# Optimization experiments

Hardware: AMD Instinct MI355X
Metric: run time of the kernel (lower is better)

Reference implementation:

```python
import jax, jax.numpy as jnp
import numpy as np
import math

D = 128       # d_model (file-scope constant)
L_LEN = 128   # length; forced == d_model by the un-transposed attention call
NH = 4        # n_head
DK = D // NH
K = 7         # depthwise conv kernel size
LC = 4        # conv_num
EPS = 1e-5    # LayerNorm eps
NEG = -1e30


def _pos_encoding():
    i = np.arange(D).astype(np.float64)
    freqs = np.where(i % 2 == 0, 10000.0 ** (-i / D), -(10000.0 ** ((1 - i) / D)))
    phases = np.where(i % 2 == 0, 0.0, math.pi / 2)
    pos = np.arange(L_LEN).astype(np.float64)[None, :]          # (1, L)
    pe = np.sin(pos * freqs[:, None] + phases[:, None])          # (D, L)
    return jnp.asarray(pe, jnp.float32)

PE = _pos_encoding()


def layernorm2d(x, w, b):
    # LayerNorm over the trailing (D, L) dims jointly, elementwise affine (D, L)
    mu = x.mean(axis=(-2, -1), keepdims=True)
    var = x.var(axis=(-2, -1), keepdims=True)
    return (x - mu) * jax.lax.rsqrt(var + EPS) * w + b


def sep_conv(x, dw_w, dw_b, pw_w, pw_b):
    # depthwise conv1d (groups=C) then 1x1 pointwise conv. x: (B, C, L)
    h = jax.lax.conv_general_dilated(
        x, dw_w[:, None, :], window_strides=(1,), padding=[(K // 2, K // 2)],
        dimension_numbers=('NCH', 'OIH', 'NCH'), feature_group_count=D)
    h = h + dw_b[:, None]
    return jnp.einsum('bcl,oc->bol', h, pw_w) + pw_b[:, None]


def mha(x, mask_f, Wq, bq, Wk, bk, Wv, bv, Wo, bo):
    # x: (B, Lx, F) with Lx == F == D here (module feeds (B, d_model, length) untransposed)
    B, Lx, _ = x.shape
    q = (x @ Wq.T + bq).reshape(B, Lx, NH, DK)
    k = (x @ Wk.T + bk).reshape(B, Lx, NH, DK)
    v = (x @ Wv.T + bv).reshape(B, Lx, NH, DK)
    scores = jnp.einsum('bqhd,bkhd->bhqk', q, k) * (1.0 / math.sqrt(DK))
    m = mask_f[:, None, None, :]                         # (B,1,1,Lx)
    scores = scores * (1.0 - m) + m * NEG                # mask_logits
    attn = jax.nn.softmax(scores, axis=-1)
    out = jnp.einsum('bhqk,bkhd->bqhd', attn, v).reshape(B, Lx, D)
    return out @ Wo.T + bo


def setup_inputs() -> dict:
    key = jax.random.key(0)
    ks = jax.random.split(key, 16)
    B = 1024
    s = 0.02
    inp = {
        'x': jax.random.normal(ks[0], (B, D, L_LEN), jnp.float32),
        'mask': jax.random.randint(ks[1], (B, L_LEN), 0, 2, jnp.int32),
        'dw_w': jax.random.normal(ks[2], (LC, D, K), jnp.float32) * s,
        'dw_b': jnp.zeros((LC, D), jnp.float32),
        'pw_w': jax.random.normal(ks[3], (LC, D, D), jnp.float32) * s,
        'pw_b': jnp.zeros((LC, D), jnp.float32),
        'normb_w': jnp.ones((D, L_LEN), jnp.float32),
        'normb_b': jnp.zeros((D, L_LEN), jnp.float32),
        'norms_w': jnp.ones((LC, D, L_LEN), jnp.float32),
        'norms_b': jnp.zeros((LC, D, L_LEN), jnp.float32),
        'norme_w': jnp.ones((D, L_LEN), jnp.float32),
        'norme_b': jnp.zeros((D, L_LEN), jnp.float32),
        'Wq': jax.random.normal(ks[4], (D, D), jnp.float32) * s,
        'bq': jnp.zeros((D,), jnp.float32),
        'Wk': jax.random.normal(ks[5], (D, D), jnp.float32) * s,
        'bk': jnp.zeros((D,), jnp.float32),
        'Wv': jax.random.normal(ks[6], (D, D), jnp.float32) * s,
        'bv': jnp.zeros((D,), jnp.float32),
        'Wo': jax.random.normal(ks[7], (D, D), jnp.float32) * s,
        'bo': jnp.zeros((D,), jnp.float32),
        'fc_w': jax.random.normal(ks[8], (D, D), jnp.float32) * s,
        'fc_b': jnp.zeros((D,), jnp.float32),
    }
    return inp


def reference(x, mask, dw_w, dw_b, pw_w, pw_b, normb_w, normb_b, norms_w, norms_b,
              norme_w, norme_b, Wq, bq, Wk, bk, Wv, bv, Wo, bo, fc_w, fc_b):
    # Eval mode: all dropouts are identity.
    mask_f = mask.astype(x.dtype)
    out = x + PE                                  # PosEncoder
    res = out
    out = layernorm2d(out, normb_w, normb_b)      # normb
    for i in range(LC):                           # fixed small layer loop
        h = sep_conv(out, dw_w[i], dw_b[i], pw_w[i], pw_b[i])
        out = jax.nn.relu(h) + res
        res = out
        out = layernorm2d(out, norms_w[i], norms_b[i])
    att = mha(out, mask_f, Wq, bq, Wk, bk, Wv, bv, Wo, bo)
    out = att + res
    res = out
    out = layernorm2d(out, norme_w, norme_b)
    # fc applied over channel dim: (B,C,L)->(B,L,C) linear ->(B,C,L)
    h = jnp.einsum('bcl,oc->bol', out, fc_w) + fc_b[:, None]
    out = jax.nn.relu(h) + res
    return out
```

## Files before the change

### kernel.cpp

```cpp
#include <hip/hip_runtime.h>

#define NEGF -1e30f
#define EPSF 1e-5f

typedef __attribute__((ext_vector_type(8))) short bf16x8;
typedef __attribute__((ext_vector_type(4))) float f32x4;
typedef unsigned short u16;
typedef unsigned int u32;

#define WSU_PW 0
#define WSU_FC 65536
#define WSU_WO 81920
#define WSU_WQ 98304
#define WSU_WK 114688
#define WSU_WV 131072
#define WSU_END 147456

__device__ __forceinline__ u16 f2bf(float x) {
  u32 u = __float_as_uint(x);
  u += 0x7fffu + ((u >> 16) & 1u);
  return (u16)(u >> 16);
}
__device__ __forceinline__ float bf2f(u16 u) {
  return __uint_as_float(((u32)u) << 16);
}
__device__ __forceinline__ f32x4 mfma16(bf16x8 a, bf16x8 b, f32x4 c) {
  return __builtin_amdgcn_mfma_f32_16x16x32_bf16(a, b, c, 0, 0, 0);
}
__device__ __forceinline__ void mm_frags(const u16* base, bf16x8* f) {
  f[0] = *(const bf16x8*)(base);
  f[1] = *(const bf16x8*)(base + 32);
  f[2] = *(const bf16x8*)(base + 64);
  f[3] = *(const bf16x8*)(base + 96);
}

__global__ __launch_bounds__(128) void prep_kernel(
    const float* __restrict__ pw_w, const float* __restrict__ fc_w,
    const float* __restrict__ Wo, const float* __restrict__ Wq,
    const float* __restrict__ Wk, const float* __restrict__ Wv,
    u16* __restrict__ wsu) {
  int job = blockIdx.x, r = blockIdx.y, c = threadIdx.x;
  int idx = r * 128 + c;
  if (job < 4)       wsu[WSU_PW + job * 16384 + idx] = f2bf(pw_w[job * 16384 + idx]);
  else if (job == 4) wsu[WSU_FC + idx] = f2bf(fc_w[idx]);
  else if (job == 5) wsu[WSU_WO + idx] = f2bf(Wo[idx]);
  else if (job == 6) wsu[WSU_WQ + idx] = f2bf(Wq[idx]);
  else if (job == 7) wsu[WSU_WK + idx] = f2bf(Wk[idx]);
  else if (job == 8) wsu[WSU_WV + idx] = f2bf(Wv[idx]);
  else {
    float* pe = (float*)(wsu + WSU_END);
    int d = r, pos = c;
    double freq, phase;
    if ((d & 1) == 0) { freq = pow(10000.0, -(double)d / 128.0); phase = 0.0; }
    else { freq = -pow(10000.0, (1.0 - (double)d) / 128.0); phase = 1.5707963267948966; }
    pe[d * 128 + pos] = (float)sin((double)pos * freq + phase);
  }
}

__device__ __forceinline__ void ln_stats(const float* resv, float* red, int t,
                                         float& mu, float& inv) {
  float s = 0.f, s2 = 0.f;
#pragma unroll
  for (int i = 0; i < 16; i++) { float v = resv[i]; s += v; s2 += v * v; }
#pragma unroll
  for (int off = 32; off > 0; off >>= 1) {
    s += __shfl_down(s, off, 64);
    s2 += __shfl_down(s2, off, 64);
  }
  if ((t & 63) == 0) { red[(t >> 6) * 2] = s; red[(t >> 6) * 2 + 1] = s2; }
  __syncthreads();
  float S = 0.f, S2 = 0.f;
#pragma unroll
  for (int i = 0; i < 16; i++) { S += red[2 * i]; S2 += red[2 * i + 1]; }
  mu = S * (1.0f / 16384.0f);
  float var = S2 * (1.0f / 16384.0f) - mu * mu;
  inv = rsqrtf(var + EPSF);
}

__global__ __launch_bounds__(1024) void enc_kernel(
    const float* __restrict__ x, const int* __restrict__ mask,
    const float* __restrict__ dw_w, const float* __restrict__ dw_b,
    const float* __restrict__ pw_b,
    const float* __restrict__ normb_w, const float* __restrict__ normb_b,
    const float* __restrict__ norms_w, const float* __restrict__ norms_b,
    const float* __restrict__ norme_w, const float* __restrict__ norme_b,
    const float* __restrict__ bq, const float* __restrict__ bk,
    const float* __restrict__ bv, const float* __restrict__ bo,
    const float* __restrict__ fc_b, const u16* __restrict__ wsu,
    const float* __restrict__ pe, float* __restrict__ out) {
  __shared__ __align__(16) u16 A_raw[128 * 136 + 16];
  __shared__ __align__(16) u16 B_[21760];
  __shared__ float mask_s[128];
  __shared__ float red[32];
  u16* A = A_raw + 8;
  u16* QH = B_;
  u16* KH = B_ + 5120;
  u16* VT = B_ + 17408;
  u16* PN = B_;

  const int t = threadIdx.x;
  const int b = blockIdx.x;
  const int lane = t & 63;
  const int r16 = lane & 15;
  const int quad = lane >> 4;
  const int wv = t >> 6;
  const int m0 = __builtin_amdgcn_readfirstlane((wv >> 1) << 4);
  const int nh = __builtin_amdgcn_readfirstlane(wv & 1);
  const int l = t & 127;
  const int og = __builtin_amdgcn_readfirstlane(t >> 7);
  const int obase = og << 4;
  const int dup = __builtin_amdgcn_readfirstlane(wv >> 3);
  const int mq0 = __builtin_amdgcn_readfirstlane((wv & 7) << 4);

  if (t < 128) mask_s[t] = (float)mask[b * 128 + t];

  float res[16];
  {
    const float* xb = x + (size_t)b * 16384;
#pragma unroll
    for (int i = 0; i < 16; i++) {
      int o = obase + i;
      res[i] = xb[o * 128 + l] + pe[o * 128 + l];
    }
  }
  {
    float mu, inv;
    ln_stats(res, red, t, mu, inv);
#pragma unroll
    for (int i = 0; i < 16; i++) {
      int o = obase + i;
      A[o * 136 + l] = f2bf((res[i] - mu) * inv * normb_w[o * 128 + l] + normb_b[o * 128 + l]);
    }
    __syncthreads();
  }

#pragma unroll 1
  for (int layer = 0; layer < 4; layer++) {
    {
      const float* dwp = dw_w + layer * 896 + l * 7;
      float wreg[7];
#pragma unroll
      for (int j = 0; j < 7; j++) wreg[j] = dwp[j];
      float bias = dw_b[layer * 128 + l];
      const u16* xrow = A + l * 136;
#pragma unroll
      for (int k = 0; k < 2; k++) {
        const int lb = (og << 4) + 8 * k;
        bf16x8 vz = {0, 0, 0, 0, 0, 0, 0, 0};
        bf16x8 vc = *(const bf16x8*)(xrow + lb);
        bf16x8 vp = (lb == 0) ? vz : *(const bf16x8*)(xrow + lb - 8);
        bf16x8 vn = (lb == 120) ? vz : *(const bf16x8*)(xrow + lb + 8);
        float w14[14];
        w14[0] = bf2f((u16)vp[5]); w14[1] = bf2f((u16)vp[6]); w14[2] = bf2f((u16)vp[7]);
#pragma unroll
        for (int j = 0; j < 8; j++) w14[3 + j] = bf2f((u16)vc[j]);
        w14[11] = bf2f((u16)vn[0]); w14[12] = bf2f((u16)vn[1]); w14[13] = bf2f((u16)vn[2]);
#pragma unroll
        for (int j = 0; j < 8; j++) {
          float a = bias;
#pragma unroll
          for (int tt = 0; tt < 7; tt++) a += w14[j + tt] * wreg[tt];
          B_[(lb + j) * 136 + l] = f2bf(a);
        }
      }
    }
    __syncthreads();
    {
      const u16* pwp = wsu + WSU_PW + (layer << 14) + (m0 + r16) * 128 + quad * 8;
      bf16x8 a[4];
      mm_frags(pwp, a);
#pragma unroll
      for (int ni = 0; ni < 4; ni++) {
        int n = nh * 4 + ni;
        const u16* hb = B_ + (16 * n + r16) * 136 + quad * 8;
        f32x4 c = {0.f, 0.f, 0.f, 0.f};
        c = mfma16(a[0], *(const bf16x8*)(hb), c);
        c = mfma16(a[1], *(const bf16x8*)(hb + 32), c);
        c = mfma16(a[2], *(const bf16x8*)(hb + 64), c);
        c = mfma16(a[3], *(const bf16x8*)(hb + 96), c);
        u16* sp = A + (m0 + quad * 4) * 136 + 16 * n + r16;
        sp[0] = f2bf(c[0]); sp[136] = f2bf(c[1]); sp[272] = f2bf(c[2]); sp[408] = f2bf(c[3]);
      }
    }
    __syncthreads();
    {
#pragma unroll
      for (int i = 0; i < 16; i++)
        res[i] += fmaxf(bf2f(A[(obase + i) * 136 + l]) + pw_b[layer * 128 + obase + i], 0.f);
      float mu, inv;
      ln_stats(res, red, t, mu, inv);
      const float* wg = norms_w + layer * 16384;
      const float* bg = norms_b + layer * 16384;
#pragma unroll
      for (int i = 0; i < 16; i++) {
        int o = obase + i;
        A[o * 136 + l] = f2bf((res[i] - mu) * inv * wg[o * 128 + l] + bg[o * 128 + l]);
      }
      __syncthreads();
    }
  }

  float att[16];
#pragma unroll
  for (int hd = 0; hd < 4; hd++) {
    {
      const u16* xp = A + (m0 + r16) * 136 + quad * 8;
      bf16x8 xf[4];
      mm_frags(xp, xf);
      const int j2 = nh * 16 + r16;
      const int jrow = hd * 32 + j2;
      {
        bf16x8 w[4];
        mm_frags(wsu + WSU_WQ + jrow * 128 + quad * 8, w);
        f32x4 c = {0.f, 0.f, 0.f, 0.f};
        c = mfma16(xf[0], w[0], c); c = mfma16(xf[1], w[1], c);
        c = mfma16(xf[2], w[2], c); c = mfma16(xf[3], w[3], c);
        float bb = bq[jrow];
#pragma unroll
        for (int r = 0; r < 4; r++)
          QH[(m0 + quad * 4 + r) * 40 + j2] = f2bf((c[r] + bb) * 0.17677669529663687f);
      }
      {
        bf16x8 w[4];
        mm_frags(wsu + WSU_WK + jrow * 128 + quad * 8, w);
        f32x4 c = {0.f, 0.f, 0.f, 0.f};
        c = mfma16(xf[0], w[0], c); c = mfma16(xf[1], w[1], c);
        c = mfma16(xf[2], w[2], c); c = mfma16(xf[3], w[3], c);
        float bb = bk[jrow];
#pragma unroll
        for (int r = 0; r < 4; r++)
          KH[(m0 + quad * 4 + r) * 40 + j2] = f2bf(c[r] + bb);
      }
      {
        bf16x8 w[4];
        mm_frags(wsu + WSU_WV + jrow * 128 + quad * 8, w);
        f32x4 c = {0.f, 0.f, 0.f, 0.f};
        c = mfma16(xf[0], w[0], c); c = mfma16(xf[1], w[1], c);
        c = mfma16(xf[2], w[2], c); c = mfma16(xf[3], w[3], c);
        float bb = bv[jrow];
        u32 lo = (u32)f2bf(c[0] + bb) | ((u32)f2bf(c[1] + bb) << 16);
        u32 hi = (u32)f2bf(c[2] + bb) | ((u32)f2bf(c[3] + bb) << 16);
        u16* vp = VT + j2 * 136 + m0 + quad * 4;
        *(u32*)(vp) = lo;
        *(u32*)(vp + 2) = hi;
      }
    }
    __syncthreads();
    f32x4 sc[8];
    {
      bf16x8 aq = *(const bf16x8*)(QH + (mq0 + r16) * 40 + quad * 8);
#pragma unroll
      for (int n = 0; n < 8; n++) {
        f32x4 z = {0.f, 0.f, 0.f, 0.f};
        sc[n] = mfma16(aq, *(const bf16x8*)(KH + (16 * n + r16) * 40 + quad * 8), z);
      }
    }
    __syncthreads();
    float linv[4];
    {
      float mv[8];
#pragma unroll
      for (int n = 0; n < 8; n++) mv[n] = mask_s[16 * n + r16];
#pragma unroll
      for (int r = 0; r < 4; r++) {
        float sv[8];
#pragma unroll
        for (int n = 0; n < 8; n++) sv[n] = (mv[n] > 0.5f) ? NEGF : sc[n][r];
        float mx = sv[0];
#pragma unroll
        for (int n = 1; n < 8; n++) mx = fmaxf(mx, sv[n]);
        mx = fmaxf(mx, __shfl_xor(mx, 1, 64));
        mx = fmaxf(mx, __shfl_xor(mx, 2, 64));
        mx = fmaxf(mx, __shfl_xor(mx, 4, 64));
        mx = fmaxf(mx, __shfl_xor(mx, 8, 64));
        float sum = 0.f;
#pragma unroll
        for (int n = 0; n < 8; n++) { float pp = __expf(sv[n] - mx); sv[n] = pp; sum += pp; }
        sum += __shfl_xor(sum, 1, 64);
        sum += __shfl_xor(sum, 2, 64);
        sum += __shfl_xor(sum, 4, 64);
        sum += __shfl_xor(sum, 8, 64);
        linv[r] = 1.0f / sum;
        u16* pp2 = PN + (mq0 + quad * 4 + r) * 136 + r16;
        if (dup == 0) {
          pp2[0] = f2bf(sv[0]); pp2[16] = f2bf(sv[1]);
          pp2[32] = f2bf(sv[2]); pp2[48] = f2bf(sv[3]);
        } else {
          pp2[64] = f2bf(sv[4]); pp2[80] = f2bf(sv[5]);
          pp2[96] = f2bf(sv[6]); pp2[112] = f2bf(sv[7]);
        }
      }
    }
    __syncthreads();
    {
      const u16* pq = PN + (mq0 + r16) * 136 + quad * 8;
      bf16x8 pf[4];
      mm_frags(pq, pf);
      const u16* vb = VT + (dup * 16 + r16) * 136 + quad * 8;
      f32x4 c = {0.f, 0.f, 0.f, 0.f};
      c = mfma16(pf[0], *(const bf16x8*)(vb), c);
      c = mfma16(pf[1], *(const bf16x8*)(vb + 32), c);
      c = mfma16(pf[2], *(const bf16x8*)(vb + 64), c);
      c = mfma16(pf[3], *(const bf16x8*)(vb + 96), c);
#pragma unroll
      for (int r = 0; r < 4; r++) att[hd * 4 + r] = c[r] * linv[r];
    }
    __syncthreads();
  }

#pragma unroll
  for (int hd = 0; hd < 4; hd++)
#pragma unroll
    for (int r = 0; r < 4; r++)
      A[(mq0 + quad * 4 + r) * 136 + hd * 32 + dup * 16 + r16] = f2bf(att[hd * 4 + r]);
  __syncthreads();
  {
    const u16* ap = A + (m0 + r16) * 136 + quad * 8;
    bf16x8 a[4];
    mm_frags(ap, a);
#pragma unroll
    for (int ni = 0; ni < 4; ni++) {
      int n = nh * 4 + ni;
      bf16x8 w[4];
      mm_frags(wsu + WSU_WO + (16 * n + r16) * 128 + quad * 8, w);
      f32x4 c = {0.f, 0.f, 0.f, 0.f};
      c = mfma16(a[0], w[0], c); c = mfma16(a[1], w[1], c);
      c = mfma16(a[2], w[2], c); c = mfma16(a[3], w[3], c);
      u16* sp = B_ + (m0 + quad * 4) * 136 + 16 * n + r16;
      sp[0] = f2bf(c[0]); sp[136] = f2bf(c[1]); sp[272] = f2bf(c[2]); sp[408] = f2bf(c[3]);
    }
  }
  __syncthreads();
  {
    float bol = bo[l];
#pragma unroll
    for (int i = 0; i < 16; i++) res[i] += bf2f(B_[(obase + i) * 136 + l]) + bol;
    float mu, inv;
    ln_stats(res, red, t, mu, inv);
#pragma unroll
    for (int i = 0; i < 16; i += 2) {
      int o = obase + i;
      float v0 = (res[i] - mu) * inv * norme_w[o * 128 + l] + norme_b[o * 128 + l];
      float v1 = (res[i + 1] - mu) * inv * norme_w[(o + 1) * 128 + l] + norme_b[(o + 1) * 128 + l];
      *(u32*)(A + l * 136 + o) = (u32)f2bf(v0) | ((u32)f2bf(v1) << 16);
    }
    __syncthreads();
  }
  {
    const u16* fp = wsu + WSU_FC + (m0 + r16) * 128 + quad * 8;
    bf16x8 a[4];
    mm_frags(fp, a);
#pragma unroll
    for (int ni = 0; ni < 4; ni++) {
      int n = nh * 4 + ni;
      const u16* hb = A + (16 * n + r16) * 136 + quad * 8;
      f32x4 c = {0.f, 0.f, 0.f, 0.f};
      c = mfma16(a[0], *(const bf16x8*)(hb), c);
      c = mfma16(a[1], *(const bf16x8*)(hb + 32), c);
      c = mfma16(a[2], *(const bf16x8*)(hb + 64), c);
      c = mfma16(a[3], *(const bf16x8*)(hb + 96), c);
      u16* sp = B_ + (m0 + quad * 4) * 136 + 16 * n + r16;
      sp[0] = f2bf(c[0]); sp[136] = f2bf(c[1]); sp[272] = f2bf(c[2]); sp[408] = f2bf(c[3]);
    }
  }
  __syncthreads();
  {
    float* outb = out + (size_t)b * 16384;
#pragma unroll
    for (int i = 0; i < 16; i++) {
      float hv = bf2f(B_[(obase + i) * 136 + l]) + fc_b[obase + i];
      outb[(obase + i) * 128 + l] = fmaxf(hv, 0.f) + res[i];
    }
  }
}

extern "C" void kernel_launch(void* const* d_in, const int* in_sizes, int n_in,
                              void* d_out, int out_size, void* d_ws, size_t ws_size,
                              hipStream_t stream) {
  const float* x       = (const float*)d_in[0];
  const int*   mask    = (const int*)d_in[1];
  const float* dw_w    = (const float*)d_in[2];
  const float* dw_b    = (const float*)d_in[3];
  const float* pw_w    = (const float*)d_in[4];
  const float* pw_b    = (const float*)d_in[5];
  const float* normb_w = (const float*)d_in[6];
  const float* normb_b = (const float*)d_in[7];
  const float* norms_w = (const float*)d_in[8];
  const float* norms_b = (const float*)d_in[9];
  const float* norme_w = (const float*)d_in[10];
  const float* norme_b = (const float*)d_in[11];
  const float* Wq      = (const float*)d_in[12];
  const float* bq      = (const float*)d_in[13];
  const float* Wk      = (const float*)d_in[14];
  const float* bk      = (const float*)d_in[15];
  const float* Wv      = (const float*)d_in[16];
  const float* bv      = (const float*)d_in[17];
  const float* Wo      = (const float*)d_in[18];
  const float* bo      = (const float*)d_in[19];
  const float* fc_w    = (const float*)d_in[20];
  const float* fc_b    = (const float*)d_in[21];
  float* out = (float*)d_out;
  u16* wsu = (u16*)d_ws;
  const float* pe = (const float*)(wsu + WSU_END);
  int B = in_sizes[0] / 16384;

  prep_kernel<<<dim3(10, 128), dim3(128), 0, stream>>>(pw_w, fc_w, Wo, Wq, Wk, Wv, wsu);
  enc_kernel<<<dim3(B), dim3(1024), 0, stream>>>(
      x, mask, dw_w, dw_b, pw_b, normb_w, normb_b, norms_w, norms_b,
      norme_w, norme_b, bq, bk, bv, bo, fc_b, wsu, pe, out);
}
```

Baseline: 615.0 us.

## Shrink LDS footprint by reusing one buffer in place and splitting softmax across waves

Drops the second large LDS buffer. Depthwise conv, pointwise, Wo and fc matmuls now write back in place into the same A buffer, with extra barriers between reading inputs into registers and storing outputs. Attention softmax is split so each wave pair handles half the keys, with cross-wave max and sum exchanged through a small LDS array. This cuts LDS use, likely to fit two 1024-thread blocks per CU. The cost is more __syncthreads, a non-unrolled head loop and extra LDS traffic for the partial statistics.

```diff
diff --git a/kernel.cpp b/kernel.cpp
--- a/kernel.cpp
+++ b/kernel.cpp
@@ -89,14 +89,14 @@
     const float* __restrict__ fc_b, const u16* __restrict__ wsu,
     const float* __restrict__ pe, float* __restrict__ out) {
   __shared__ __align__(16) u16 A_raw[128 * 136 + 16];
-  __shared__ __align__(16) u16 B_[21760];
+  __shared__ __align__(16) u16 VTb[32 * 136];
+  __shared__ float EX[512];
   __shared__ float mask_s[128];
   __shared__ float red[32];
   u16* A = A_raw + 8;
-  u16* QH = B_;
-  u16* KH = B_ + 5120;
-  u16* VT = B_ + 17408;
-  u16* PN = B_;
+  u16* QH = A;
+  u16* KH = A + 5120;
+  u16* PN = A;
 
   const int t = threadIdx.x;
   const int b = blockIdx.x;
@@ -143,24 +143,30 @@
       for (int j = 0; j < 7; j++) wreg[j] = dwp[j];
       float bias = dw_b[layer * 128 + l];
       const u16* xrow = A + l * 136;
+      const int lb = og << 4;
+      bf16x8 vz = {0, 0, 0, 0, 0, 0, 0, 0};
+      bf16x8 v0 = (lb == 0) ? vz : *(const bf16x8*)(xrow + lb - 8);
+      bf16x8 v1 = *(const bf16x8*)(xrow + lb);
+      bf16x8 v2 = *(const bf16x8*)(xrow + lb + 8);
+      bf16x8 v3 = (lb == 112) ? vz : *(const bf16x8*)(xrow + lb + 16);
+      __syncthreads();
 #pragma unroll
       for (int k = 0; k < 2; k++) {
-        const int lb = (og << 4) + 8 * k;
-        bf16x8 vz = {0, 0, 0, 0, 0, 0, 0, 0};
-        bf16x8 vc = *(const bf16x8*)(xrow + lb);
-        bf16x8 vp = (lb == 0) ? vz : *(const bf16x8*)(xrow + lb - 8);
-        bf16x8 vn = (lb == 120) ? vz : *(const bf16x8*)(xrow + lb + 8);
+        bf16x8 vp = k ? v1 : v0;
+        bf16x8 vc = k ? v2 : v1;
+        bf16x8 vn = k ? v3 : v2;
         float w14[14];
         w14[0] = bf2f((u16)vp[5]); w14[1] = bf2f((u16)vp[6]); w14[2] = bf2f((u16)vp[7]);
 #pragma unroll
         for (int j = 0; j < 8; j++) w14[3 + j] = bf2f((u16)vc[j]);
         w14[11] = bf2f((u16)vn[0]); w14[12] = bf2f((u16)vn[1]); w14[13] = bf2f((u16)vn[2]);
+        const int lb2 = lb + 8 * k;
 #pragma unroll
         for (int j = 0; j < 8; j++) {
           float a = bias;
 #pragma unroll
           for (int tt = 0; tt < 7; tt++) a += w14[j + tt] * wreg[tt];
-          B_[(lb + j) * 136 + l] = f2bf(a);
+          A[(lb2 + j) * 136 + l] = f2bf(a);
         }
       }
     }
@@ -169,17 +175,25 @@
       const u16* pwp = wsu + WSU_PW + (layer << 14) + (m0 + r16) * 128 + quad * 8;
       bf16x8 a[4];
       mm_frags(pwp, a);
+      f32x4 c4[4];
 #pragma unroll
       for (int ni = 0; ni < 4; ni++) {
         int n = nh * 4 + ni;
-        const u16* hb = B_ + (16 * n + r16) * 136 + quad * 8;
+        const u16* hb = A + (16 * n + r16) * 136 + quad * 8;
         f32x4 c = {0.f, 0.f, 0.f, 0.f};
         c = mfma16(a[0], *(const bf16x8*)(hb), c);
         c = mfma16(a[1], *(const bf16x8*)(hb + 32), c);
         c = mfma16(a[2], *(const bf16x8*)(hb + 64), c);
         c = mfma16(a[3], *(const bf16x8*)(hb + 96), c);
+        c4[ni] = c;
+      }
+      __syncthreads();
+#pragma unroll
+      for (int ni = 0; ni < 4; ni++) {
+        int n = nh * 4 + ni;
         u16* sp = A + (m0 + quad * 4) * 136 + 16 * n + r16;
-        sp[0] = f2bf(c[0]); sp[136] = f2bf(c[1]); sp[272] = f2bf(c[2]); sp[408] = f2bf(c[3]);
+        sp[0] = f2bf(c4[ni][0]); sp[136] = f2bf(c4[ni][1]);
+        sp[272] = f2bf(c4[ni][2]); sp[408] = f2bf(c4[ni][3]);
       }
     }
     __syncthreads();
@@ -200,13 +214,14 @@
     }
   }
 
-  float att[16];
-#pragma unroll
+  bf16x8 xf[4];
+  mm_frags(A + (m0 + r16) * 136 + quad * 8, xf);
+  __syncthreads();
+
+  u32 att32[8];
+#pragma unroll 1
   for (int hd = 0; hd < 4; hd++) {
     {
-      const u16* xp = A + (m0 + r16) * 136 + quad * 8;
-      bf16x8 xf[4];
-      mm_frags(xp, xf);
       const int j2 = nh * 16 + r16;
       const int jrow = hd * 32 + j2;
       {
@@ -240,70 +255,73 @@
         float bb = bv[jrow];
         u32 lo = (u32)f2bf(c[0] + bb) | ((u32)f2bf(c[1] + bb) << 16);
         u32 hi = (u32)f2bf(c[2] + bb) | ((u32)f2bf(c[3] + bb) << 16);
-        u16* vp = VT + j2 * 136 + m0 + quad * 4;
+        u16* vp = VTb + j2 * 136 + m0 + quad * 4;
         *(u32*)(vp) = lo;
         *(u32*)(vp + 2) = hi;
       }
     }
     __syncthreads();
-    f32x4 sc[8];
+    f32x4 sc[4];
     {
       bf16x8 aq = *(const bf16x8*)(QH + (mq0 + r16) * 40 + quad * 8);
 #pragma unroll
-      for (int n = 0; n < 8; n++) {
+      for (int ni = 0; ni < 4; ni++) {
         f32x4 z = {0.f, 0.f, 0.f, 0.f};
-        sc[n] = mfma16(aq, *(const bf16x8*)(KH + (16 * n + r16) * 40 + quad * 8), z);
-      }
-    }
-    __syncthreads();
-    float linv[4];
-    {
-      float mv[8];
-#pragma unroll
-      for (int n = 0; n < 8; n++) mv[n] = mask_s[16 * n + r16];
-#pragma unroll
-      for (int r = 0; r < 4; r++) {
-        float sv[8];
-#pragma unroll
-        for (int n = 0; n < 8; n++) sv[n] = (mv[n] > 0.5f) ? NEGF : sc[n][r];
-        float mx = sv[0];
-#pragma unroll
-        for (int n = 1; n < 8; n++) mx = fmaxf(mx, sv[n]);
-        mx = fmaxf(mx, __shfl_xor(mx, 1, 64));
-        mx = fmaxf(mx, __shfl_xor(mx, 2, 64));
-        mx = fmaxf(mx, __shfl_xor(mx, 4, 64));
-        mx = fmaxf(mx, __shfl_xor(mx, 8, 64));
-        float sum = 0.f;
-#pragma unroll
-        for (int n = 0; n < 8; n++) { float pp = __expf(sv[n] - mx); sv[n] = pp; sum += pp; }
-        sum += __shfl_xor(sum, 1, 64);
-        sum += __shfl_xor(sum, 2, 64);
-        sum += __shfl_xor(sum, 4, 64);
-        sum += __shfl_xor(sum, 8, 64);
-        linv[r] = 1.0f / sum;
-        u16* pp2 = PN + (mq0 + quad * 4 + r) * 136 + r16;
-        if (dup == 0) {
-          pp2[0] = f2bf(sv[0]); pp2[16] = f2bf(sv[1]);
-          pp2[32] = f2bf(sv[2]); pp2[48] = f2bf(sv[3]);
-        } else {
-          pp2[64] = f2bf(sv[4]); pp2[80] = f2bf(sv[5]);
-          pp2[96] = f2bf(sv[6]); pp2[112] = f2bf(sv[7]);
-        }
-      }
+        sc[ni] = mfma16(aq, *(const bf16x8*)(KH + ((dup * 4 + ni) * 16 + r16) * 40 + quad * 8), z);
+      }
+#pragma unroll
+      for (int ni = 0; ni < 4; ni++) {
+        float mv = mask_s[(dup * 4 + ni) * 16 + r16];
+        if (mv > 0.5f) { sc[ni][0] = NEGF; sc[ni][1] = NEGF; sc[ni][2] = NEGF; sc[ni][3] = NEGF; }
+      }
+    }
+    float mxr[4];
+#pragma unroll
+    for (int r = 0; r < 4; r++) {
+      float mx = fmaxf(fmaxf(sc[0][r], sc[1][r]), fmaxf(sc[2][r], sc[3][r]));
+      mx = fmaxf(mx, __shfl_xor(mx, 1, 64));
+      mx = fmaxf(mx, __shfl_xor(mx, 2, 64));
+      mx = fmaxf(mx, __shfl_xor(mx, 4, 64));
+      mx = fmaxf(mx, __shfl_xor(mx, 8, 64));
+      if (r16 == 0) EX[dup * 128 + mq0 + quad * 4 + r] = mx;
+      mxr[r] = mx;
+    }
+    __syncthreads();
+    float ps[4];
+#pragma unroll
+    for (int r = 0; r < 4; r++) {
+      const int row = mq0 + quad * 4 + r;
+      float fm = fmaxf(mxr[r], EX[(dup ^ 1) * 128 + row]);
+      float s = 0.f;
+      u16* pp2 = PN + row * 136 + r16;
+#pragma unroll
+      for (int ni = 0; ni < 4; ni++) {
+        float p = __expf(sc[ni][r] - fm);
+        pp2[(dup * 4 + ni) * 16] = f2bf(p);
+        s += p;
+      }
+      s += __shfl_xor(s, 1, 64);
+      s += __shfl_xor(s, 2, 64);
+      s += __shfl_xor(s, 4, 64);
+      s += __shfl_xor(s, 8, 64);
+      if (r16 == 0) EX[256 + dup * 128 + row] = s;
+      ps[r] = s;
     }
     __syncthreads();
     {
       const u16* pq = PN + (mq0 + r16) * 136 + quad * 8;
-      bf16x8 pf[4];
-      mm_frags(pq, pf);
-      const u16* vb = VT + (dup * 16 + r16) * 136 + quad * 8;
+      const u16* vb = VTb + (dup * 16 + r16) * 136 + quad * 8;
       f32x4 c = {0.f, 0.f, 0.f, 0.f};
-      c = mfma16(pf[0], *(const bf16x8*)(vb), c);
-      c = mfma16(pf[1], *(const bf16x8*)(vb + 32), c);
-      c = mfma16(pf[2], *(const bf16x8*)(vb + 64), c);
-      c = mfma16(pf[3], *(const bf16x8*)(vb + 96), c);
-#pragma unroll
-      for (int r = 0; r < 4; r++) att[hd * 4 + r] = c[r] * linv[r];
+      c = mfma16(*(const bf16x8*)(pq), *(const bf16x8*)(vb), c);
+      c = mfma16(*(const bf16x8*)(pq + 32), *(const bf16x8*)(vb + 32), c);
+      c = mfma16(*(const bf16x8*)(pq + 64), *(const bf16x8*)(vb + 64), c);
+      c = mfma16(*(const bf16x8*)(pq + 96), *(const bf16x8*)(vb + 96), c);
+      float v0 = c[0] / (ps[0] + EX[256 + (dup ^ 1) * 128 + mq0 + quad * 4 + 0]);
+      float v1 = c[1] / (ps[1] + EX[256 + (dup ^ 1) * 128 + mq0 + quad * 4 + 1]);
+      float v2 = c[2] / (ps[2] + EX[256 + (dup ^ 1) * 128 + mq0 + quad * 4 + 2]);
+      float v3 = c[3] / (ps[3] + EX[256 + (dup ^ 1) * 128 + mq0 + quad * 4 + 3]);
+      att32[hd * 2 + 0] = (u32)f2bf(v0) | ((u32)f2bf(v1) << 16);
+      att32[hd * 2 + 1] = (u32)f2bf(v2) | ((u32)f2bf(v3) << 16);
     }
     __syncthreads();
   }
@@ -311,30 +329,41 @@
 #pragma unroll
   for (int hd = 0; hd < 4; hd++)
 #pragma unroll
-    for (int r = 0; r < 4; r++)
-      A[(mq0 + quad * 4 + r) * 136 + hd * 32 + dup * 16 + r16] = f2bf(att[hd * 4 + r]);
+    for (int i = 0; i < 2; i++)
+#pragma unroll
+      for (int h = 0; h < 2; h++)
+        A[(mq0 + quad * 4 + 2 * i + h) * 136 + hd * 32 + dup * 16 + r16] =
+            (u16)(att32[hd * 2 + i] >> (16 * h));
   __syncthreads();
   {
     const u16* ap = A + (m0 + r16) * 136 + quad * 8;
-    bf16x8 a[4];
-    mm_frags(ap, a);
+    bf16x8 a4[4];
+    mm_frags(ap, a4);
+    f32x4 c4[4];
 #pragma unroll
     for (int ni = 0; ni < 4; ni++) {
       int n = nh * 4 + ni;
       bf16x8 w[4];
       mm_frags(wsu + WSU_WO + (16 * n + r16) * 128 + quad * 8, w);
       f32x4 c = {0.f, 0.f, 0.f, 0.f};
-      c = mfma16(a[0], w[0], c); c = mfma16(a[1], w[1], c);
-      c = mfma16(a[2], w[2], c); c = mfma16(a[3], w[3], c);
-      u16* sp = B_ + (m0 + quad * 4) * 136 + 16 * n + r16;
-      sp[0] = f2bf(c[0]); sp[136] = f2bf(c[1]); sp[272] = f2bf(c[2]); sp[408] = f2bf(c[3]);
+      c = mfma16(a4[0], w[0], c); c = mfma16(a4[1], w[1], c);
+      c = mfma16(a4[2], w[2], c); c = mfma16(a4[3], w[3], c);
+      c4[ni] = c;
+    }
+    __syncthreads();
+#pragma unroll
+    for (int ni = 0; ni < 4; ni++) {
+      int n = nh * 4 + ni;
+      u16* sp = A + (m0 + quad * 4) * 136 + 16 * n + r16;
+      sp[0] = f2bf(c4[ni][0]); sp[136] = f2bf(c4[ni][1]);
+      sp[272] = f2bf(c4[ni][2]); sp[408] = f2bf(c4[ni][3]);
     }
   }
   __syncthreads();
   {
     float bol = bo[l];
 #pragma unroll
-    for (int i = 0; i < 16; i++) res[i] += bf2f(B_[(obase + i) * 136 + l]) + bol;
+    for (int i = 0; i < 16; i++) res[i] += bf2f(A[(obase + i) * 136 + l]) + bol;
     float mu, inv;
     ln_stats(res, red, t, mu, inv);
 #pragma unroll
@@ -348,19 +377,27 @@
   }
   {
     const u16* fp = wsu + WSU_FC + (m0 + r16) * 128 + quad * 8;
-    bf16x8 a[4];
-    mm_frags(fp, a);
+    bf16x8 a4[4];
+    mm_frags(fp, a4);
+    f32x4 c4[4];
 #pragma unroll
     for (int ni = 0; ni < 4; ni++) {
       int n = nh * 4 + ni;
       const u16* hb = A + (16 * n + r16) * 136 + quad * 8;
       f32x4 c = {0.f, 0.f, 0.f, 0.f};
-      c = mfma16(a[0], *(const bf16x8*)(hb), c);
-      c = mfma16(a[1], *(const bf16x8*)(hb + 32), c);
-      c = mfma16(a[2], *(const bf16x8*)(hb + 64), c);
-      c = mfma16(a[3], *(const bf16x8*)(hb + 96), c);
-      u16* sp = B_ + (m0 + quad * 4) * 136 + 16 * n + r16;
-      sp[0] = f2bf(c[0]); sp[136] = f2bf(c[1]); sp[272] = f2bf(c[2]); sp[408] = f2bf(c[3]);
+      c = mfma16(a4[0], *(const bf16x8*)(hb), c);
+      c = mfma16(a4[1], *(const bf16x8*)(hb + 32), c);
+      c = mfma16(a4[2], *(const bf16x8*)(hb + 64), c);
+      c = mfma16(a4[3], *(const bf16x8*)(hb + 96), c);
+      c4[ni] = c;
+    }
+    __syncthreads();
+#pragma unroll
+    for (int ni = 0; ni < 4; ni++) {
+      int n = nh * 4 + ni;
+      u16* sp = A + (m0 + quad * 4) * 136 + 16 * n + r16;
+      sp[0] = f2bf(c4[ni][0]); sp[136] = f2bf(c4[ni][1]);
+      sp[272] = f2bf(c4[ni][2]); sp[408] = f2bf(c4[ni][3]);
     }
   }
   __syncthreads();
@@ -368,7 +405,7 @@
     float* outb = out + (size_t)b * 16384;
 #pragma unroll
     for (int i = 0; i < 16; i++) {
-      float hv = bf2f(B_[(obase + i) * 136 + l]) + fc_b[obase + i];
+      float hv = bf2f(A[(obase + i) * 136 + l]) + fc_b[obase + i];
       outb[(obase + i) * 128 + l] = fmaxf(hv, 0.f) + res[i];
     }
   }
```

Result: slower. 644.4 us (+4.8%).

## Halve block size and reuse one LDS buffer to fit more blocks per CU

Applied to the files above, without the earlier changes.

Each block now runs 512 threads instead of 1024, with each thread holding 32 residual values and each wave computing full 16x128 output tiles. The second large shared buffer is removed: depthwise conv, pointwise/fc GEMM outputs, Q/K and probabilities all reuse the A buffer in place, with extra barriers and register-held accumulators. Only a small V^T buffer is kept. The goal is lower LDS per block so several blocks can be co-resident per CU, at the cost of higher register pressure and more barriers per block.

```diff
diff --git a/kernel.cpp b/kernel.cpp
--- a/kernel.cpp
+++ b/kernel.cpp
@@ -57,11 +57,11 @@
   }
 }
 
-__device__ __forceinline__ void ln_stats(const float* resv, float* red, int t,
-                                         float& mu, float& inv) {
+__device__ __forceinline__ void ln_stats8(const float* resv, float* red, int t,
+                                          float& mu, float& inv) {
   float s = 0.f, s2 = 0.f;
 #pragma unroll
-  for (int i = 0; i < 16; i++) { float v = resv[i]; s += v; s2 += v * v; }
+  for (int i = 0; i < 32; i++) { float v = resv[i]; s += v; s2 += v * v; }
 #pragma unroll
   for (int off = 32; off > 0; off >>= 1) {
     s += __shfl_down(s, off, 64);
@@ -71,13 +71,13 @@
   __syncthreads();
   float S = 0.f, S2 = 0.f;
 #pragma unroll
-  for (int i = 0; i < 16; i++) { S += red[2 * i]; S2 += red[2 * i + 1]; }
+  for (int i = 0; i < 8; i++) { S += red[2 * i]; S2 += red[2 * i + 1]; }
   mu = S * (1.0f / 16384.0f);
   float var = S2 * (1.0f / 16384.0f) - mu * mu;
   inv = rsqrtf(var + EPSF);
 }
 
-__global__ __launch_bounds__(1024) void enc_kernel(
+__global__ __launch_bounds__(512, 4) void enc_kernel(
     const float* __restrict__ x, const int* __restrict__ mask,
     const float* __restrict__ dw_w, const float* __restrict__ dw_b,
     const float* __restrict__ pw_b,
@@ -89,14 +89,13 @@
     const float* __restrict__ fc_b, const u16* __restrict__ wsu,
     const float* __restrict__ pe, float* __restrict__ out) {
   __shared__ __align__(16) u16 A_raw[128 * 136 + 16];
-  __shared__ __align__(16) u16 B_[21760];
+  __shared__ __align__(16) u16 VTb[32 * 136];
   __shared__ float mask_s[128];
-  __shared__ float red[32];
+  __shared__ float red[16];
   u16* A = A_raw + 8;
-  u16* QH = B_;
-  u16* KH = B_ + 5120;
-  u16* VT = B_ + 17408;
-  u16* PN = B_;
+  u16* QH = A;
+  u16* KH = A + 5120;
+  u16* PN = A;
 
   const int t = threadIdx.x;
   const int b = blockIdx.x;
@@ -104,30 +103,27 @@
   const int r16 = lane & 15;
   const int quad = lane >> 4;
   const int wv = t >> 6;
-  const int m0 = __builtin_amdgcn_readfirstlane((wv >> 1) << 4);
-  const int nh = __builtin_amdgcn_readfirstlane(wv & 1);
+  const int m0 = __builtin_amdgcn_readfirstlane(wv << 4);
   const int l = t & 127;
   const int og = __builtin_amdgcn_readfirstlane(t >> 7);
-  const int obase = og << 4;
-  const int dup = __builtin_amdgcn_readfirstlane(wv >> 3);
-  const int mq0 = __builtin_amdgcn_readfirstlane((wv & 7) << 4);
+  const int obase = og << 5;
 
   if (t < 128) mask_s[t] = (float)mask[b * 128 + t];
 
-  float res[16];
+  float res[32];
   {
     const float* xb = x + (size_t)b * 16384;
 #pragma unroll
-    for (int i = 0; i < 16; i++) {
+    for (int i = 0; i < 32; i++) {
       int o = obase + i;
       res[i] = xb[o * 128 + l] + pe[o * 128 + l];
     }
   }
   {
     float mu, inv;
-    ln_stats(res, red, t, mu, inv);
-#pragma unroll
-    for (int i = 0; i < 16; i++) {
+    ln_stats8(res, red, t, mu, inv);
+#pragma unroll
+    for (int i = 0; i < 32; i++) {
       int o = obase + i;
       A[o * 136 + l] = f2bf((res[i] - mu) * inv * normb_w[o * 128 + l] + normb_b[o * 128 + l]);
     }
@@ -143,56 +139,69 @@
       for (int j = 0; j < 7; j++) wreg[j] = dwp[j];
       float bias = dw_b[layer * 128 + l];
       const u16* xrow = A + l * 136;
-#pragma unroll
-      for (int k = 0; k < 2; k++) {
-        const int lb = (og << 4) + 8 * k;
-        bf16x8 vz = {0, 0, 0, 0, 0, 0, 0, 0};
-        bf16x8 vc = *(const bf16x8*)(xrow + lb);
-        bf16x8 vp = (lb == 0) ? vz : *(const bf16x8*)(xrow + lb - 8);
-        bf16x8 vn = (lb == 120) ? vz : *(const bf16x8*)(xrow + lb + 8);
+      const int lb = og << 5;
+      bf16x8 vz = {0, 0, 0, 0, 0, 0, 0, 0};
+      bf16x8 vm = (lb == 0) ? vz : *(const bf16x8*)(xrow + lb - 8);
+      bf16x8 v0 = *(const bf16x8*)(xrow + lb);
+      bf16x8 v1 = *(const bf16x8*)(xrow + lb + 8);
+      bf16x8 v2 = *(const bf16x8*)(xrow + lb + 16);
+      bf16x8 v3 = *(const bf16x8*)(xrow + lb + 24);
+      bf16x8 vp = (lb == 96) ? vz : *(const bf16x8*)(xrow + lb + 32);
+      __syncthreads();
+#pragma unroll
+      for (int g = 0; g < 4; g++) {
+        bf16x8 pv = (g == 0) ? vm : ((g == 1) ? v0 : ((g == 2) ? v1 : v2));
+        bf16x8 cv = (g == 0) ? v0 : ((g == 1) ? v1 : ((g == 2) ? v2 : v3));
+        bf16x8 nv = (g == 0) ? v1 : ((g == 1) ? v2 : ((g == 2) ? v3 : vp));
         float w14[14];
-        w14[0] = bf2f((u16)vp[5]); w14[1] = bf2f((u16)vp[6]); w14[2] = bf2f((u16)vp[7]);
-#pragma unroll
-        for (int j = 0; j < 8; j++) w14[3 + j] = bf2f((u16)vc[j]);
-        w14[11] = bf2f((u16)vn[0]); w14[12] = bf2f((u16)vn[1]); w14[13] = bf2f((u16)vn[2]);
+        w14[0] = bf2f((u16)pv[5]); w14[1] = bf2f((u16)pv[6]); w14[2] = bf2f((u16)pv[7]);
+#pragma unroll
+        for (int j = 0; j < 8; j++) w14[3 + j] = bf2f((u16)cv[j]);
+        w14[11] = bf2f((u16)nv[0]); w14[12] = bf2f((u16)nv[1]); w14[13] = bf2f((u16)nv[2]);
+        const int lb2 = lb + 8 * g;
 #pragma unroll
         for (int j = 0; j < 8; j++) {
           float a = bias;
 #pragma unroll
           for (int tt = 0; tt < 7; tt++) a += w14[j + tt] * wreg[tt];
-          B_[(lb + j) * 136 + l] = f2bf(a);
+          A[(lb2 + j) * 136 + l] = f2bf(a);
         }
       }
     }
     __syncthreads();
     {
-      const u16* pwp = wsu + WSU_PW + (layer << 14) + (m0 + r16) * 128 + quad * 8;
-      bf16x8 a[4];
-      mm_frags(pwp, a);
-#pragma unroll
-      for (int ni = 0; ni < 4; ni++) {
-        int n = nh * 4 + ni;
-        const u16* hb = B_ + (16 * n + r16) * 136 + quad * 8;
+      bf16x8 a4[4];
+      mm_frags(wsu + WSU_PW + (layer << 14) + (m0 + r16) * 128 + quad * 8, a4);
+      f32x4 acc[8];
+#pragma unroll
+      for (int n = 0; n < 8; n++) {
+        const u16* hb = A + (16 * n + r16) * 136 + quad * 8;
         f32x4 c = {0.f, 0.f, 0.f, 0.f};
-        c = mfma16(a[0], *(const bf16x8*)(hb), c);
-        c = mfma16(a[1], *(const bf16x8*)(hb + 32), c);
-        c = mfma16(a[2], *(const bf16x8*)(hb + 64), c);
-        c = mfma16(a[3], *(const bf16x8*)(hb + 96), c);
+        c = mfma16(a4[0], *(const bf16x8*)(hb), c);
+        c = mfma16(a4[1], *(const bf16x8*)(hb + 32), c);
+        c = mfma16(a4[2], *(const bf16x8*)(hb + 64), c);
+        c = mfma16(a4[3], *(const bf16x8*)(hb + 96), c);
+        acc[n] = c;
+      }
+      __syncthreads();
+#pragma unroll
+      for (int n = 0; n < 8; n++) {
         u16* sp = A + (m0 + quad * 4) * 136 + 16 * n + r16;
-        sp[0] = f2bf(c[0]); sp[136] = f2bf(c[1]); sp[272] = f2bf(c[2]); sp[408] = f2bf(c[3]);
-      }
-    }
-    __syncthreads();
-    {
-#pragma unroll
-      for (int i = 0; i < 16; i++)
+        sp[0] = f2bf(acc[n][0]); sp[136] = f2bf(acc[n][1]);
+        sp[272] = f2bf(acc[n][2]); sp[408] = f2bf(acc[n][3]);
+      }
+    }
+    __syncthreads();
+    {
+#pragma unroll
+      for (int i = 0; i < 32; i++)
         res[i] += fmaxf(bf2f(A[(obase + i) * 136 + l]) + pw_b[layer * 128 + obase + i], 0.f);
       float mu, inv;
-      ln_stats(res, red, t, mu, inv);
+      ln_stats8(res, red, t, mu, inv);
       const float* wg = norms_w + layer * 16384;
       const float* bg = norms_b + layer * 16384;
 #pragma unroll
-      for (int i = 0; i < 16; i++) {
+      for (int i = 0; i < 32; i++) {
         int o = obase + i;
         A[o * 136 + l] = f2bf((res[i] - mu) * inv * wg[o * 128 + l] + bg[o * 128 + l]);
       }
@@ -200,14 +209,16 @@
     }
   }
 
-  float att[16];
+  bf16x8 xf[4];
+  mm_frags(A + (m0 + r16) * 136 + quad * 8, xf);
+  __syncthreads();
+
+  u32 att32[16];
 #pragma unroll
   for (int hd = 0; hd < 4; hd++) {
-    {
-      const u16* xp = A + (m0 + r16) * 136 + quad * 8;
-      bf16x8 xf[4];
-      mm_frags(xp, xf);
-      const int j2 = nh * 16 + r16;
+#pragma unroll
+    for (int jt = 0; jt < 2; jt++) {
+      const int j2 = jt * 16 + r16;
       const int jrow = hd * 32 + j2;
       {
         bf16x8 w[4];
@@ -238,17 +249,15 @@
         c = mfma16(xf[0], w[0], c); c = mfma16(xf[1], w[1], c);
         c = mfma16(xf[2], w[2], c); c = mfma16(xf[3], w[3], c);
         float bb = bv[jrow];
-        u32 lo = (u32)f2bf(c[0] + bb) | ((u32)f2bf(c[1] + bb) << 16);
-        u32 hi = (u32)f2bf(c[2] + bb) | ((u32)f2bf(c[3] + bb) << 16);
-        u16* vp = VT + j2 * 136 + m0 + quad * 4;
-        *(u32*)(vp) = lo;
-        *(u32*)(vp + 2) = hi;
+        u16* vp = VTb + j2 * 136 + m0 + quad * 4;
+        *(u32*)(vp) = (u32)f2bf(c[0] + bb) | ((u32)f2bf(c[1] + bb) << 16);
+        *(u32*)(vp + 2) = (u32)f2bf(c[2] + bb) | ((u32)f2bf(c[3] + bb) << 16);
       }
     }
     __syncthreads();
     f32x4 sc[8];
     {
-      bf16x8 aq = *(const bf16x8*)(QH + (mq0 + r16) * 40 + quad * 8);
+      bf16x8 aq = *(const bf16x8*)(QH + (m0 + r16) * 40 + quad * 8);
 #pragma unroll
       for (int n = 0; n < 8; n++) {
         f32x4 z = {0.f, 0.f, 0.f, 0.f};
@@ -281,29 +290,29 @@
         sum += __shfl_xor(sum, 4, 64);
         sum += __shfl_xor(sum, 8, 64);
         linv[r] = 1.0f / sum;
-        u16* pp2 = PN + (mq0 + quad * 4 + r) * 136 + r16;
-        if (dup == 0) {
-          pp2[0] = f2bf(sv[0]); pp2[16] = f2bf(sv[1]);
-          pp2[32] = f2bf(sv[2]); pp2[48] = f2bf(sv[3]);
-        } else {
-          pp2[64] = f2bf(sv[4]); pp2[80] = f2bf(sv[5]);
-          pp2[96] = f2bf(sv[6]); pp2[112] = f2bf(sv[7]);
-        }
-      }
-    }
-    __syncthreads();
-    {
-      const u16* pq = PN + (mq0 + r16) * 136 + quad * 8;
+        u16* pp2 = PN + (m0 + quad * 4 + r) * 136 + r16;
+#pragma unroll
+        for (int n = 0; n < 8; n++) pp2[16 * n] = f2bf(sv[n]);
+      }
+    }
+    __syncthreads();
+    {
+      const u16* pq = PN + (m0 + r16) * 136 + quad * 8;
       bf16x8 pf[4];
       mm_frags(pq, pf);
-      const u16* vb = VT + (dup * 16 + r16) * 136 + quad * 8;
-      f32x4 c = {0.f, 0.f, 0.f, 0.f};
-      c = mfma16(pf[0], *(const bf16x8*)(vb), c);
-      c = mfma16(pf[1], *(const bf16x8*)(vb + 32), c);
-      c = mfma16(pf[2], *(const bf16x8*)(vb + 64), c);
-      c = mfma16(pf[3], *(const bf16x8*)(vb + 96), c);
-#pragma unroll
-      for (int r = 0; r < 4; r++) att[hd * 4 + r] = c[r] * linv[r];
+#pragma unroll
+      for (int nv = 0; nv < 2; nv++) {
+        const u16* vb = VTb + (nv * 16 + r16) * 136 + quad * 8;
+        f32x4 c = {0.f, 0.f, 0.f, 0.f};
+        c = mfma16(pf[0], *(const bf16x8*)(vb), c);
+        c = mfma16(pf[1], *(const bf16x8*)(vb + 32), c);
+        c = mfma16(pf[2], *(const bf16x8*)(vb + 64), c);
+        c = mfma16(pf[3], *(const bf16x8*)(vb + 96), c);
+        float v0 = c[0] * linv[0], v1 = c[1] * linv[1];
+        float v2 = c[2] * linv[2], v3 = c[3] * linv[3];
+        att32[hd * 4 + nv * 2 + 0] = (u32)f2bf(v0) | ((u32)f2bf(v1) << 16);
+        att32[hd * 4 + nv * 2 + 1] = (u32)f2bf(v2) | ((u32)f2bf(v3) << 16);
+      }
     }
     __syncthreads();
   }
@@ -311,22 +320,26 @@
 #pragma unroll
   for (int hd = 0; hd < 4; hd++)
 #pragma unroll
-    for (int r = 0; r < 4; r++)
-      A[(mq0 + quad * 4 + r) * 136 + hd * 32 + dup * 16 + r16] = f2bf(att[hd * 4 + r]);
+    for (int nv = 0; nv < 2; nv++) {
+      int col = hd * 32 + nv * 16 + r16;
+      u32 lo = att32[hd * 4 + nv * 2 + 0], hi = att32[hd * 4 + nv * 2 + 1];
+      A[(m0 + quad * 4 + 0) * 136 + col] = (u16)(lo);
+      A[(m0 + quad * 4 + 1) * 136 + col] = (u16)(lo >> 16);
+      A[(m0 + quad * 4 + 2) * 136 + col] = (u16)(hi);
+      A[(m0 + quad * 4 + 3) * 136 + col] = (u16)(hi >> 16);
+    }
   __syncthreads();
   {
-    const u16* ap = A + (m0 + r16) * 136 + quad * 8;
-    bf16x8 a[4];
-    mm_frags(ap, a);
-#pragma unroll
-    for (int ni = 0; ni < 4; ni++) {
-      int n = nh * 4 + ni;
+    bf16x8 a4[4];
+    mm_frags(A + (m0 + r16) * 136 + quad * 8, a4);
+#pragma unroll
+    for (int n = 0; n < 8; n++) {
       bf16x8 w[4];
       mm_frags(wsu + WSU_WO + (16 * n + r16) * 128 + quad * 8, w);
       f32x4 c = {0.f, 0.f, 0.f, 0.f};
-      c = mfma16(a[0], w[0], c); c = mfma16(a[1], w[1], c);
-      c = mfma16(a[2], w[2], c); c = mfma16(a[3], w[3], c);
-      u16* sp = B_ + (m0 + quad * 4) * 136 + 16 * n + r16;
+      c = mfma16(a4[0], w[0], c); c = mfma16(a4[1], w[1], c);
+      c = mfma16(a4[2], w[2], c); c = mfma16(a4[3], w[3], c);
+      u16* sp = A + (m0 + quad * 4) * 136 + 16 * n + r16;
       sp[0] = f2bf(c[0]); sp[136] = f2bf(c[1]); sp[272] = f2bf(c[2]); sp[408] = f2bf(c[3]);
     }
   }
@@ -334,11 +347,11 @@
   {
     float bol = bo[l];
 #pragma unroll
-    for (int i = 0; i < 16; i++) res[i] += bf2f(B_[(obase + i) * 136 + l]) + bol;
+    for (int i = 0; i < 32; i++) res[i] += bf2f(A[(obase + i) * 136 + l]) + bol;
     float mu, inv;
-    ln_stats(res, red, t, mu, inv);
-#pragma unroll
-    for (int i = 0; i < 16; i += 2) {
+    ln_stats8(res, red, t, mu, inv);
+#pragma unroll
+    for (int i = 0; i < 32; i += 2) {
       int o = obase + i;
       float v0 = (res[i] - mu) * inv * norme_w[o * 128 + l] + norme_b[o * 128 + l];
       float v1 = (res[i + 1] - mu) * inv * norme_w[(o + 1) * 128 + l] + norme_b[(o + 1) * 128 + l];
@@ -347,29 +360,35 @@
     __syncthreads();
   }
   {
-    const u16* fp = wsu + WSU_FC + (m0 + r16) * 128 + quad * 8;
-    bf16x8 a[4];
-    mm_frags(fp, a);
-#pragma unroll
-    for (int ni = 0; ni < 4; ni++) {
-      int n = nh * 4 + ni;
+    bf16x8 a4[4];
+    mm_frags(wsu + WSU_FC + (m0 + r16) * 128 + quad * 8, a4);
+    f32x4 acc[8];
+#pragma unroll
+    for (int n = 0; n < 8; n++) {
       const u16* hb = A + (16 * n + r16) * 136 + quad * 8;
       f32x4 c = {0.f, 0.f, 0.f, 0.f};
-      c = mfma16(a[0], *(const bf16x8*)(hb), c);
-      c = mfma16(a[1], *(const bf16x8*)(hb + 32), c);
-      c = mfma16(a[2], *(const bf16x8*)(hb + 64), c);
-      c = mfma16(a[3], *(const bf16x8*)(hb + 96), c);
-      u16* sp = B_ + (m0 + quad * 4) * 136 + 16 * n + r16;
-      sp[0] = f2bf(c[0]); sp[136] = f2bf(c[1]); sp[272] = f2bf(c[2]); sp[408] = f2bf(c[3]);
+      c = mfma16(a4[0], *(const bf16x8*)(hb), c);
+      c = mfma16(a4[1], *(const bf16x8*)(hb + 32), c);
+      c = mfma16(a4[2], *(const bf16x8*)(hb + 64), c);
+      c = mfma16(a4[3], *(const bf16x8*)(hb + 96), c);
+      acc[n] = c;
+    }
+    __syncthreads();
+#pragma unroll
+    for (int n = 0; n < 8; n++) {
+      u16* sp = A + (m0 + quad * 4) * 136 + 16 * n + r16;
+      sp[0] = f2bf(acc[n][0]); sp[136] = f2bf(acc[n][1]);
+      sp[272] = f2bf(acc[n][2]); sp[408] = f2bf(acc[n][3]);
     }
   }
   __syncthreads();
   {
     float* outb = out + (size_t)b * 16384;
 #pragma unroll
-    for (int i = 0; i < 16; i++) {
-      float hv = bf2f(B_[(obase + i) * 136 + l]) + fc_b[obase + i];
-      outb[(obase + i) * 128 + l] = fmaxf(hv, 0.f) + res[i];
+    for (int i = 0; i < 32; i++) {
+      int o = obase + i;
+      float hv = bf2f(A[o * 136 + l]) + fc_b[o];
+      outb[o * 128 + l] = fmaxf(hv, 0.f) + res[i];
     }
   }
 }
@@ -405,7 +424,7 @@
   int B = in_sizes[0] / 16384;
 
   prep_kernel<<<dim3(10, 128), dim3(128), 0, stream>>>(pw_w, fc_w, Wo, Wq, Wk, Wv, wsu);
-  enc_kernel<<<dim3(B), dim3(1024), 0, stream>>>(
+  enc_kernel<<<dim3(B), dim3(512), 0, stream>>>(
       x, mask, dw_w, dw_b, pw_b, normb_w, normb_b, norms_w, norms_b,
       norme_w, norme_b, bq, bk, bv, bo, fc_b, wsu, pe, out);
 }
```

Measured after the change: 713.5 us. +16.0%, slower.
